# Optimization experiments

Hardware: AMD Instinct MI355X
Metric: run time of the kernel (lower is better)

Reference implementation:

```python
import jax, jax.numpy as jnp
import numpy as np

NEG_SLOPE = 0.2

def gat_conv(x, W, a_src, a_dst, bias, src, dst, num_nodes, concat):
    # x: [N, F_in]; W: [F_in, H*C]; a_src/a_dst: [H, C]; src/dst: [E] (self-loops included)
    H, C = a_src.shape
    h = (x @ W).reshape(-1, H, C)                      # [N, H, C]
    alpha_s = jnp.einsum('nhc,hc->nh', h, a_src)       # [N, H]
    alpha_d = jnp.einsum('nhc,hc->nh', h, a_dst)       # [N, H]
    e = jax.nn.leaky_relu(alpha_s[src] + alpha_d[dst], NEG_SLOPE)  # [E, H]
    # segment softmax over destination nodes
    m = jax.ops.segment_max(e, dst, num_segments=num_nodes)        # [N, H]
    ex = jnp.exp(e - m[dst])
    denom = jax.ops.segment_sum(ex, dst, num_segments=num_nodes)   # [N, H]
    alpha = ex / (denom[dst] + 1e-16)                  # [E, H]
    msg = alpha[:, :, None] * h[src]                   # [E, H, C]
    out = jax.ops.segment_sum(msg, dst, num_segments=num_nodes)    # [N, H, C]
    if concat:
        out = out.reshape(num_nodes, H * C)
    else:
        out = out.mean(axis=1)
    return out + bias

def setup_inputs() -> dict:
    key = jax.random.key(0)
    ks = jax.random.split(key, 12)
    N, F_in, E = 100000, 512, 3200000
    H1, C1 = 8, 8
    OUT = 40
    x = jax.random.normal(ks[0], (N, F_in), dtype=jnp.float32)
    edge_index = jax.random.randint(ks[1], (2, E), 0, N, dtype=jnp.int64)
    glorot = lambda k, shape: jax.random.uniform(k, shape, jnp.float32, -1.0, 1.0) * np.sqrt(6.0 / (shape[0] + shape[-1]))
    W1 = glorot(ks[2], (F_in, H1 * C1))
    a_src1 = glorot(ks[3], (H1, C1))
    a_dst1 = glorot(ks[4], (H1, C1))
    b1 = jnp.zeros((H1 * C1,), jnp.float32)
    W2 = glorot(ks[5], (H1 * C1, OUT))
    a_src2 = glorot(ks[6], (1, OUT))
    a_dst2 = glorot(ks[7], (1, OUT))
    b2 = jnp.zeros((OUT,), jnp.float32)
    return {"x": x, "edge_index": edge_index, "W1": W1, "a_src1": a_src1,
            "a_dst1": a_dst1, "b1": b1, "W2": W2, "a_src2": a_src2,
            "a_dst2": a_dst2, "b2": b2}

def reference(x, edge_index, W1, a_src1, a_dst1, b1, W2, a_src2, a_dst2, b2):
    N = x.shape[0]
    loop = jnp.arange(N, dtype=edge_index.dtype)
    src = jnp.concatenate([edge_index[0], loop])  # add_self_loops=True (PyG default)
    dst = jnp.concatenate([edge_index[1], loop])
    # dropout is identity in eval mode
    h = gat_conv(x, W1, a_src1, a_dst1, b1, src, dst, N, concat=True)   # [N, 64]
    h = jax.nn.elu(h)
    out = gat_conv(h, W2, a_src2, a_dst2, b2, src, dst, N, concat=False)  # [N, 40]
    return out
```

## Files before the change

### kernel.cpp

```cpp
#include <hip/hip_runtime.h>
#include <hip/hip_bf16.h>


typedef __attribute__((ext_vector_type(8))) short short8;
typedef __attribute__((ext_vector_type(4))) short short4v;
typedef __attribute__((ext_vector_type(4))) float float4v;

#define NEG_SLOPE 0.2f

static __device__ __forceinline__ short f2bf(float v){
    union { float f; unsigned u; } x; x.f = v;
    unsigned r = x.u + 0x7fffu + ((x.u >> 16) & 1u);
    return (short)(r >> 16);
}
static __device__ __forceinline__ float bf2f(short s){
    union { unsigned u; float f; } x; x.u = ((unsigned)(unsigned short)s) << 16;
    return x.f;
}

__global__ void pack_w1(const float* __restrict__ W1, short* __restrict__ Bhi, short* __restrict__ Blo){
    int idx = blockIdx.x*blockDim.x + threadIdx.x;
    if (idx >= 64*512) return;
    int j    = idx & 7;
    int lane = (idx >> 3) & 63;
    int ct   = (idx >> 9) & 3;
    int tks  = idx >> 11;
    int ks = tks & 1, t = tks >> 1;
    int m = lane & 15, q = lane >> 4;
    int n = ct*16 + m;
    int k = t*64 + ks*32 + q*8 + j;
    float w = W1[k*64 + n];
    short h = f2bf(w);
    Bhi[idx] = h;
    Blo[idx] = f2bf(w - bf2f(h));
}

__global__ void detect_i64(const int* __restrict__ ei, int* __restrict__ flag){
    __shared__ int any;
    if (threadIdx.x == 0) any = 0;
    __syncthreads();
    if (ei[2*threadIdx.x + 1] != 0) atomicAdd(&any, 1);
    __syncthreads();
    if (threadIdx.x == 0) flag[0] = (any == 0) ? 1 : 0;
}

__global__ __launch_bounds__(256, 4) void gemm1(const float* __restrict__ x,
        const short* __restrict__ Bhi, const short* __restrict__ Blo,
        const float* __restrict__ aS1, const float* __restrict__ aD1,
        short* __restrict__ h1b, float* __restrict__ as1, float* __restrict__ ad1, int N){
    __shared__ __align__(16) float As[2][64][68];
    int tid = threadIdx.x;
    int wave = tid >> 6, lane = tid & 63;
    int m = lane & 15, q = lane >> 4;
    int rowbase = blockIdx.x*64;

    const short8* Bh = (const short8*)Bhi;
    const short8* Bl = (const short8*)Blo;

    int srow[4]; int scol[4];
    #pragma unroll
    for (int i = 0; i < 4; ++i){
        int f = i*256 + tid;
        int r = rowbase + (f >> 4);
        srow[i] = (r < N) ? r : (N-1);
        scol[i] = (f & 15) * 4;
    }

    float4 reg[4];
    #pragma unroll
    for (int i = 0; i < 4; ++i)
        reg[i] = *(const float4*)(x + (size_t)srow[i]*512 + scol[i]);
    #pragma unroll
    for (int i = 0; i < 4; ++i){
        int f = i*256 + tid;
        *(float4*)&As[0][f >> 4][scol[i]] = reg[i];
    }
    __syncthreads();

    float4v acc[4] = {};
    for (int t = 0; t < 8; ++t){
        int cur = t & 1;
        if (t < 7){
            #pragma unroll
            for (int i = 0; i < 4; ++i)
                reg[i] = *(const float4*)(x + (size_t)srow[i]*512 + (t+1)*64 + scol[i]);
        }
        const float* arow = &As[cur][wave*16 + m][0];
        #pragma unroll
        for (int ks = 0; ks < 2; ++ks){
            float v[8];
            *(float4*)&v[0] = *(const float4*)(arow + ks*32 + q*8);
            *(float4*)&v[4] = *(const float4*)(arow + ks*32 + q*8 + 4);
            short8 ahi, alo;
            #pragma unroll
            for (int j = 0; j < 8; ++j){
                union { float f; unsigned u; } tt; tt.f = v[j];
                ahi[j] = (short)(tt.u >> 16);
                union { unsigned u; float f; } th; th.u = tt.u & 0xffff0000u;
                alo[j] = f2bf(v[j] - th.f);
            }
            int fb = ((t*2 + ks)*4)*64 + lane;
            #pragma unroll
            for (int ct = 0; ct < 4; ++ct){
                short8 bhi = Bh[fb + ct*64];
                short8 blo = Bl[fb + ct*64];
                acc[ct] = __builtin_amdgcn_mfma_f32_16x16x32_bf16(ahi, bhi, acc[ct], 0, 0, 0);
                acc[ct] = __builtin_amdgcn_mfma_f32_16x16x32_bf16(ahi, blo, acc[ct], 0, 0, 0);
                acc[ct] = __builtin_amdgcn_mfma_f32_16x16x32_bf16(alo, bhi, acc[ct], 0, 0, 0);
            }
        }
        if (t < 7){
            #pragma unroll
            for (int i = 0; i < 4; ++i){
                int f = i*256 + tid;
                *(float4*)&As[t & 1 ? 0 : 1][f >> 4][scol[i]] = reg[i];
            }
            __syncthreads();
        }
    }

    float* cw = &As[0][0][0] + wave*(16*68);
    #pragma unroll
    for (int ct = 0; ct < 4; ++ct)
        #pragma unroll
        for (int r = 0; r < 4; ++r)
            cw[(q*4+r)*68 + ct*16 + m] = acc[ct][r];

    int row_l = lane >> 2;
    int cseg  = (lane & 3) * 16;
    int gr = rowbase + wave*16 + row_l;
    float vals[16];
    #pragma unroll
    for (int i = 0; i < 4; ++i)
        *(float4*)&vals[i*4] = *(const float4*)&cw[row_l*68 + cseg + i*4];
    if (gr < N){
        short8 o0, o1;
        #pragma unroll
        for (int j = 0; j < 8; ++j){ o0[j] = f2bf(vals[j]); o1[j] = f2bf(vals[8+j]); }
        *(short8*)&h1b[(size_t)gr*64 + cseg]     = o0;
        *(short8*)&h1b[(size_t)gr*64 + cseg + 8] = o1;
        int h0 = (lane & 3) * 2;
        float s0 = 0.f, d0 = 0.f, s1 = 0.f, d1 = 0.f;
        #pragma unroll
        for (int c = 0; c < 8; ++c){
            s0 = fmaf(vals[c],   aS1[h0*8+c],     s0);
            d0 = fmaf(vals[c],   aD1[h0*8+c],     d0);
            s1 = fmaf(vals[8+c], aS1[(h0+1)*8+c], s1);
            d1 = fmaf(vals[8+c], aD1[(h0+1)*8+c], d1);
        }
        float2 sv; sv.x = s0; sv.y = s1;
        float2 dv; dv.x = d0; dv.y = d1;
        *(float2*)&as1[(size_t)gr*8 + h0] = sv;
        *(float2*)&ad1[(size_t)gr*8 + h0] = dv;
    }
}

__global__ __launch_bounds__(256) void bucket_hist(const int* __restrict__ ei,
        const int* __restrict__ flag, int* __restrict__ bhist, int E, int Etot, int K){
    extern __shared__ int hist[];
    for (int i = threadIdx.x; i < K; i += 256) hist[i] = 0;
    __syncthreads();
    int f = flag[0];
    int e0 = blockIdx.x*8192, e1 = min(e0 + 8192, Etot);
    for (int e = e0 + threadIdx.x; e < e1; e += 256){
        int dst = (e < E) ? ei[((size_t)(E + e)) << f] : (e - E);
        atomicAdd(&hist[dst >> 8], 1);
    }
    __syncthreads();
    for (int i = threadIdx.x; i < K; i += 256)
        if (hist[i]) atomicAdd(&bhist[i], hist[i]);
}

__global__ __launch_bounds__(1024) void bucket_scan(const int* __restrict__ bhist,
        int* __restrict__ bbase, int* __restrict__ bcursor, int K){
    __shared__ int s[1024];
    int t = threadIdx.x;
    int v = (t < K) ? bhist[t] : 0;
    s[t] = v; __syncthreads();
    for (int off = 1; off < 1024; off <<= 1){
        int x = (t >= off) ? s[t-off] : 0;
        __syncthreads();
        s[t] += x;
        __syncthreads();
    }
    if (t < K){ int excl = s[t] - v; bbase[t] = excl; bcursor[t] = excl; }
    if (t == K) bbase[K] = s[t];
}

__global__ __launch_bounds__(256) void bucket_place(const int* __restrict__ ei,
        const int* __restrict__ flag, int* __restrict__ bcursor,
        int* __restrict__ staging, int E, int Etot, int K){
    extern __shared__ int sm[];
    int* hist = sm;
    int* base = sm + K;
    for (int i = threadIdx.x; i < K; i += 256) hist[i] = 0;
    __syncthreads();
    int f = flag[0];
    int e0 = blockIdx.x*8192, e1 = min(e0 + 8192, Etot);
    for (int e = e0 + threadIdx.x; e < e1; e += 256){
        int dst = (e < E) ? ei[((size_t)(E + e)) << f] : (e - E);
        atomicAdd(&hist[dst >> 8], 1);
    }
    __syncthreads();
    for (int i = threadIdx.x; i < K; i += 256){
        int c = hist[i];
        base[i] = c ? atomicAdd(&bcursor[i], c) : 0;
        hist[i] = 0;
    }
    __syncthreads();
    for (int e = e0 + threadIdx.x; e < e1; e += 256){
        int src, dst;
        if (e < E){ src = ei[((size_t)e) << f]; dst = ei[((size_t)(E + e)) << f]; }
        else      { src = dst = e - E; }
        int k = dst >> 8;
        int r = atomicAdd(&hist[k], 1);
        staging[base[k] + r] = (src << 8) | (dst & 255);
    }
}

__global__ __launch_bounds__(256) void bucket_csr(const int* __restrict__ staging,
        const int* __restrict__ bbase, int* __restrict__ offs, int* __restrict__ deg,
        int* __restrict__ csr, int N, int K){
    __shared__ int dcnt[256], sc[256], cur[256];
    int k = blockIdx.x, t = threadIdx.x;
    dcnt[t] = 0;
    __syncthreads();
    int s0 = bbase[k], s1 = bbase[k+1];
    for (int i = s0 + t; i < s1; i += 256)
        atomicAdd(&dcnt[staging[i] & 255], 1);
    __syncthreads();
    int v = dcnt[t];
    sc[t] = v; __syncthreads();
    for (int off = 1; off < 256; off <<= 1){
        int x = (t >= off) ? sc[t-off] : 0;
        __syncthreads();
        sc[t] += x;
        __syncthreads();
    }
    int excl = sc[t] - v;
    int node = (k << 8) + t;
    if (node < N){ offs[node] = s0 + excl; deg[node] = v; }
    cur[t] = excl;
    __syncthreads();
    for (int i = s0 + t; i < s1; i += 256){
        int ent = staging[i];
        int p = atomicAdd(&cur[ent & 255], 1);
        csr[s0 + p] = ent >> 8;
    }
}

__global__ __launch_bounds__(256) void agg1(const short* __restrict__ h1b,
        const float* __restrict__ as1, const float* __restrict__ ad1,
        const int* __restrict__ offs, const int* __restrict__ deg, const int* __restrict__ csr,
        const float* __restrict__ b1, short* __restrict__ x1b, int N){
    int w = blockIdx.x*4 + (threadIdx.x >> 6);
    if (w >= N) return;
    int lane = threadIdx.x & 63, h = lane >> 3;
    int s0 = offs[w], d = deg[w];
    float ad = ad1[w*8 + h];
    float l = 0.f, acc = 0.f;
    int i = 0;
    for (; i + 4 <= d; i += 4){
        int sa = csr[s0+i], sb = csr[s0+i+1], sc = csr[s0+i+2], sd = csr[s0+i+3];
        float ea = as1[sa*8+h], eb = as1[sb*8+h], ec = as1[sc*8+h], ed = as1[sd*8+h];
        float va = bf2f(h1b[(size_t)sa*64 + lane]);
        float vb = bf2f(h1b[(size_t)sb*64 + lane]);
        float vc = bf2f(h1b[(size_t)sc*64 + lane]);
        float vd = bf2f(h1b[(size_t)sd*64 + lane]);
        ea += ad; ea = (ea > 0.f) ? ea : NEG_SLOPE*ea; float pa = __expf(ea);
        eb += ad; eb = (eb > 0.f) ? eb : NEG_SLOPE*eb; float pb = __expf(eb);
        ec += ad; ec = (ec > 0.f) ? ec : NEG_SLOPE*ec; float pc = __expf(ec);
        ed += ad; ed = (ed > 0.f) ? ed : NEG_SLOPE*ed; float pd = __expf(ed);
        l += (pa + pb) + (pc + pd);
        acc = fmaf(pa, va, acc); acc = fmaf(pb, vb, acc);
        acc = fmaf(pc, vc, acc); acc = fmaf(pd, vd, acc);
    }
    for (; i < d; ++i){
        int s = csr[s0 + i];
        float e = as1[s*8 + h] + ad;
        e = (e > 0.f) ? e : NEG_SLOPE*e;
        float p = __expf(e);
        l += p;
        acc = fmaf(p, bf2f(h1b[(size_t)s*64 + lane]), acc);
    }
    float o = acc/(l + 1e-16f) + b1[lane];
    o = (o > 0.f) ? o : (__expf(o) - 1.f);
    x1b[(size_t)w*64 + lane] = f2bf(o);
}

__global__ __launch_bounds__(256) void gemm2a(const short* __restrict__ x1b,
        const float* __restrict__ W2, const float* __restrict__ aS2, const float* __restrict__ aD2,
        short* __restrict__ h2b, float* __restrict__ as2, float* __restrict__ ad2, int N){
    __shared__ float w2s[64*40];
    __shared__ float xs[4][64];
    int tid = threadIdx.x;
    for (int i = tid; i < 64*40; i += 256) w2s[i] = W2[i];
    int wv = tid >> 6, lane = tid & 63;
    int n = blockIdx.x*4 + wv;
    bool valid = n < N;
    if (valid && lane < 16){
        short4v xv = *(const short4v*)&x1b[(size_t)n*64 + lane*4];
        xs[wv][lane*4+0] = bf2f(xv[0]);
        xs[wv][lane*4+1] = bf2f(xv[1]);
        xs[wv][lane*4+2] = bf2f(xv[2]);
        xs[wv][lane*4+3] = bf2f(xv[3]);
    }
    __syncthreads();
    int c = (lane < 40) ? lane : 39;
    float acc = 0.f;
    #pragma unroll 8
    for (int k = 0; k < 64; ++k)
        acc = fmaf(xs[wv][k], w2s[k*40 + c], acc);
    float s = (lane < 40) ? acc * aS2[lane] : 0.f;
    float d = (lane < 40) ? acc * aD2[lane] : 0.f;
    #pragma unroll
    for (int off = 32; off > 0; off >>= 1){ s += __shfl_down(s, off, 64); d += __shfl_down(d, off, 64); }
    if (valid){
        if (lane < 40) h2b[(size_t)n*40 + lane] = f2bf(acc);
        if (lane == 0){ as2[n] = s; ad2[n] = d; }
    }
}

__global__ __launch_bounds__(256) void agg2(const short* __restrict__ h2b,
        const float* __restrict__ as2, const float* __restrict__ ad2,
        const int* __restrict__ offs, const int* __restrict__ deg, const int* __restrict__ csr,
        const float* __restrict__ b2, float* __restrict__ out, int N){
    int w = blockIdx.x*4 + (threadIdx.x >> 6);
    if (w >= N) return;
    int lane = threadIdx.x & 63;
    int c = (lane < 40) ? lane : 0;
    int s0 = offs[w], d = deg[w];
    float ad = ad2[w];
    float l = 0.f, acc = 0.f;
    int i = 0;
    for (; i + 4 <= d; i += 4){
        int sa = csr[s0+i], sb = csr[s0+i+1], sc = csr[s0+i+2], sd = csr[s0+i+3];
        float ea = as2[sa], eb = as2[sb], ec = as2[sc], ed = as2[sd];
        float va = bf2f(h2b[(size_t)sa*40 + c]);
        float vb = bf2f(h2b[(size_t)sb*40 + c]);
        float vc = bf2f(h2b[(size_t)sc*40 + c]);
        float vd = bf2f(h2b[(size_t)sd*40 + c]);
        ea += ad; ea = (ea > 0.f) ? ea : NEG_SLOPE*ea; float pa = __expf(ea);
        eb += ad; eb = (eb > 0.f) ? eb : NEG_SLOPE*eb; float pb = __expf(eb);
        ec += ad; ec = (ec > 0.f) ? ec : NEG_SLOPE*ec; float pc = __expf(ec);
        ed += ad; ed = (ed > 0.f) ? ed : NEG_SLOPE*ed; float pd = __expf(ed);
        l += (pa + pb) + (pc + pd);
        acc = fmaf(pa, va, acc); acc = fmaf(pb, vb, acc);
        acc = fmaf(pc, vc, acc); acc = fmaf(pd, vd, acc);
    }
    for (; i < d; ++i){
        int s = csr[s0 + i];
        float e = as2[s] + ad;
        e = (e > 0.f) ? e : NEG_SLOPE*e;
        float p = __expf(e);
        l += p;
        acc = fmaf(p, bf2f(h2b[(size_t)s*40 + c]), acc);
    }
    if (lane < 40) out[(size_t)w*40 + lane] = acc/(l + 1e-16f) + b2[lane];
}

extern "C" void kernel_launch(void* const* d_in, const int* in_sizes, int n_in,
                              void* d_out, int out_size, void* d_ws, size_t ws_size,
                              hipStream_t stream) {
    const float* x    = (const float*)d_in[0];
    const int*   ei   = (const int*)d_in[1];
    const float* W1   = (const float*)d_in[2];
    const float* aS1  = (const float*)d_in[3];
    const float* aD1  = (const float*)d_in[4];
    const float* b1   = (const float*)d_in[5];
    const float* W2   = (const float*)d_in[6];
    const float* aS2  = (const float*)d_in[7];
    const float* aD2  = (const float*)d_in[8];
    const float* b2   = (const float*)d_in[9];
    float* out = (float*)d_out;

    const int N    = in_sizes[0] / 512;
    const int E    = in_sizes[1] / 2;
    const int Etot = E + N;
    const int K    = (N + 255) >> 8;
    const int nAB  = (Etot + 8191) / 8192;

    char* p = (char*)d_ws;
    auto carve = [&](size_t bytes)->char*{ char* q = p; p += ((bytes + 255) & ~(size_t)255); return q; };
    short* h1b   = (short*)carve((size_t)N*64*2);
    short* x1b   = (short*)carve((size_t)N*64*2);
    short* h2b   = (short*)carve((size_t)N*40*2);
    float* as1   = (float*)carve((size_t)N*8*4);
    float* ad1   = (float*)carve((size_t)N*8*4);
    float* as2   = (float*)carve((size_t)N*4);
    float* ad2   = (float*)carve((size_t)N*4);
    int*   deg   = (int*)carve((size_t)N*4);
    int*   offs  = (int*)carve((size_t)N*4);
    int*   bhist = (int*)carve((size_t)(K+1)*4);
    int*   bbase = (int*)carve((size_t)(K+1)*4);
    int*   bcursor=(int*)carve((size_t)(K+1)*4);
    int*   flag  = (int*)carve(256);
    short* Bhi   = (short*)carve(64*512*2);
    short* Blo   = (short*)carve(64*512*2);
    int*   csr   = (int*)carve((size_t)Etot*4);
    int*   staging = (int*)carve((size_t)Etot*4);

    hipMemsetAsync(bhist, 0, (size_t)K*4, stream);

    detect_i64<<<1, 1024, 0, stream>>>(ei, flag);
    pack_w1<<<(64*512 + 255)/256, 256, 0, stream>>>(W1, Bhi, Blo);

    bucket_hist <<<nAB, 256, (size_t)K*4,   stream>>>(ei, flag, bhist, E, Etot, K);
    bucket_scan <<<1, 1024, 0,              stream>>>(bhist, bbase, bcursor, K);
    bucket_place<<<nAB, 256, (size_t)2*K*4, stream>>>(ei, flag, bcursor, staging, E, Etot, K);
    bucket_csr  <<<K, 256, 0,               stream>>>(staging, bbase, offs, deg, csr, N, K);

    gemm1 <<<(N + 63)/64, 256, 0, stream>>>(x, Bhi, Blo, aS1, aD1, h1b, as1, ad1, N);

    agg1  <<<(N + 3)/4,  256, 0, stream>>>(h1b, as1, ad1, offs, deg, csr, b1, x1b, N);
    gemm2a<<<(N + 3)/4,  256, 0, stream>>>(x1b, W2, aS2, aD2, h2b, as2, ad2, N);
    agg2  <<<(N + 3)/4,  256, 0, stream>>>(h2b, as2, ad2, offs, deg, csr, b2, out, N);
}
```

Before: 783.1 us.

## Process each destination node with 16 lanes using 4-wide bf16 vector gathers

Both aggregation kernels now assign 16 threads per destination node instead of a full 64-lane wavefront, with each thread loading four bf16 features at once (short4v) and keeping four accumulators. This puts four nodes in each wavefront, so the per-edge index loads, attention-score loads and exp work are spread over more nodes per instruction and idle lanes in the 40-wide second layer are reduced. The trade-off is more registers per thread and a wider spread of per-wavefront degree, since the wave's loop runs until its highest-degree node is done.

Measured after the change: 696.4 us. -11.1%, faster.

```diff
diff --git a/kernel.cpp b/kernel.cpp
--- a/kernel.cpp
+++ b/kernel.cpp
@@ -253,39 +253,56 @@
         const float* __restrict__ as1, const float* __restrict__ ad1,
         const int* __restrict__ offs, const int* __restrict__ deg, const int* __restrict__ csr,
         const float* __restrict__ b1, short* __restrict__ x1b, int N){
-    int w = blockIdx.x*4 + (threadIdx.x >> 6);
-    if (w >= N) return;
-    int lane = threadIdx.x & 63, h = lane >> 3;
-    int s0 = offs[w], d = deg[w];
-    float ad = ad1[w*8 + h];
-    float l = 0.f, acc = 0.f;
-    int i = 0;
-    for (; i + 4 <= d; i += 4){
-        int sa = csr[s0+i], sb = csr[s0+i+1], sc = csr[s0+i+2], sd = csr[s0+i+3];
-        float ea = as1[sa*8+h], eb = as1[sb*8+h], ec = as1[sc*8+h], ed = as1[sd*8+h];
-        float va = bf2f(h1b[(size_t)sa*64 + lane]);
-        float vb = bf2f(h1b[(size_t)sb*64 + lane]);
-        float vc = bf2f(h1b[(size_t)sc*64 + lane]);
-        float vd = bf2f(h1b[(size_t)sd*64 + lane]);
-        ea += ad; ea = (ea > 0.f) ? ea : NEG_SLOPE*ea; float pa = __expf(ea);
-        eb += ad; eb = (eb > 0.f) ? eb : NEG_SLOPE*eb; float pb = __expf(eb);
-        ec += ad; ec = (ec > 0.f) ? ec : NEG_SLOPE*ec; float pc = __expf(ec);
-        ed += ad; ed = (ed > 0.f) ? ed : NEG_SLOPE*ed; float pd = __expf(ed);
-        l += (pa + pb) + (pc + pd);
-        acc = fmaf(pa, va, acc); acc = fmaf(pb, vb, acc);
-        acc = fmaf(pc, vc, acc); acc = fmaf(pd, vd, acc);
-    }
-    for (; i < d; ++i){
-        int s = csr[s0 + i];
-        float e = as1[s*8 + h] + ad;
-        e = (e > 0.f) ? e : NEG_SLOPE*e;
-        float p = __expf(e);
-        l += p;
-        acc = fmaf(p, bf2f(h1b[(size_t)s*64 + lane]), acc);
-    }
-    float o = acc/(l + 1e-16f) + b1[lane];
-    o = (o > 0.f) ? o : (__expf(o) - 1.f);
-    x1b[(size_t)w*64 + lane] = f2bf(o);
+    int w = blockIdx.x*16 + (threadIdx.x >> 4);
+    if (w < N){
+        int r = threadIdx.x & 15;
+        int h = r >> 1;
+        int f0 = r*4;
+        int s0 = offs[w], d = deg[w];
+        float ad = ad1[w*8 + h];
+        float l = 0.f;
+        float4v acc = {};
+        int i = 0;
+        for (; i + 4 <= d; i += 4){
+            int sa = csr[s0+i], sb = csr[s0+i+1], sc = csr[s0+i+2], sd = csr[s0+i+3];
+            float ea = as1[sa*8+h], eb = as1[sb*8+h], ec = as1[sc*8+h], ed = as1[sd*8+h];
+            short4v va = *(const short4v*)&h1b[(size_t)sa*64 + f0];
+            short4v vb = *(const short4v*)&h1b[(size_t)sb*64 + f0];
+            short4v vc = *(const short4v*)&h1b[(size_t)sc*64 + f0];
+            short4v vd = *(const short4v*)&h1b[(size_t)sd*64 + f0];
+            ea += ad; ea = (ea > 0.f) ? ea : NEG_SLOPE*ea; float pa = __expf(ea);
+            eb += ad; eb = (eb > 0.f) ? eb : NEG_SLOPE*eb; float pb = __expf(eb);
+            ec += ad; ec = (ec > 0.f) ? ec : NEG_SLOPE*ec; float pc = __expf(ec);
+            ed += ad; ed = (ed > 0.f) ? ed : NEG_SLOPE*ed; float pd = __expf(ed);
+            l += (pa + pb) + (pc + pd);
+            #pragma unroll
+            for (int j = 0; j < 4; ++j){
+                acc[j] = fmaf(pa, bf2f(va[j]), acc[j]);
+                acc[j] = fmaf(pb, bf2f(vb[j]), acc[j]);
+                acc[j] = fmaf(pc, bf2f(vc[j]), acc[j]);
+                acc[j] = fmaf(pd, bf2f(vd[j]), acc[j]);
+            }
+        }
+        for (; i < d; ++i){
+            int s = csr[s0 + i];
+            float e = as1[s*8 + h] + ad;
+            e = (e > 0.f) ? e : NEG_SLOPE*e;
+            float p = __expf(e);
+            l += p;
+            short4v v = *(const short4v*)&h1b[(size_t)s*64 + f0];
+            #pragma unroll
+            for (int j = 0; j < 4; ++j)
+                acc[j] = fmaf(p, bf2f(v[j]), acc[j]);
+        }
+        short4v o;
+        #pragma unroll
+        for (int j = 0; j < 4; ++j){
+            float ov = acc[j]/(l + 1e-16f) + b1[f0+j];
+            ov = (ov > 0.f) ? ov : (__expf(ov) - 1.f);
+            o[j] = f2bf(ov);
+        }
+        *(short4v*)&x1b[(size_t)w*64 + f0] = o;
+    }
 }
 
 __global__ __launch_bounds__(256) void gemm2a(const short* __restrict__ x1b,
@@ -325,38 +342,56 @@
         const float* __restrict__ as2, const float* __restrict__ ad2,
         const int* __restrict__ offs, const int* __restrict__ deg, const int* __restrict__ csr,
         const float* __restrict__ b2, float* __restrict__ out, int N){
-    int w = blockIdx.x*4 + (threadIdx.x >> 6);
-    if (w >= N) return;
-    int lane = threadIdx.x & 63;
-    int c = (lane < 40) ? lane : 0;
-    int s0 = offs[w], d = deg[w];
-    float ad = ad2[w];
-    float l = 0.f, acc = 0.f;
-    int i = 0;
-    for (; i + 4 <= d; i += 4){
-        int sa = csr[s0+i], sb = csr[s0+i+1], sc = csr[s0+i+2], sd = csr[s0+i+3];
-        float ea = as2[sa], eb = as2[sb], ec = as2[sc], ed = as2[sd];
-        float va = bf2f(h2b[(size_t)sa*40 + c]);
-        float vb = bf2f(h2b[(size_t)sb*40 + c]);
-        float vc = bf2f(h2b[(size_t)sc*40 + c]);
-        float vd = bf2f(h2b[(size_t)sd*40 + c]);
-        ea += ad; ea = (ea > 0.f) ? ea : NEG_SLOPE*ea; float pa = __expf(ea);
-        eb += ad; eb = (eb > 0.f) ? eb : NEG_SLOPE*eb; float pb = __expf(eb);
-        ec += ad; ec = (ec > 0.f) ? ec : NEG_SLOPE*ec; float pc = __expf(ec);
-        ed += ad; ed = (ed > 0.f) ? ed : NEG_SLOPE*ed; float pd = __expf(ed);
-        l += (pa + pb) + (pc + pd);
-        acc = fmaf(pa, va, acc); acc = fmaf(pb, vb, acc);
-        acc = fmaf(pc, vc, acc); acc = fmaf(pd, vd, acc);
-    }
-    for (; i < d; ++i){
-        int s = csr[s0 + i];
-        float e = as2[s] + ad;
-        e = (e > 0.f) ? e : NEG_SLOPE*e;
-        float p = __expf(e);
-        l += p;
-        acc = fmaf(p, bf2f(h2b[(size_t)s*40 + c]), acc);
-    }
-    if (lane < 40) out[(size_t)w*40 + lane] = acc/(l + 1e-16f) + b2[lane];
+    int w = blockIdx.x*16 + (threadIdx.x >> 4);
+    if (w < N){
+        int r = threadIdx.x & 15;
+        bool pay = r < 10;
+        int f0 = pay ? r*4 : 0;
+        int s0 = offs[w], d = deg[w];
+        float ad = ad2[w];
+        float l = 0.f;
+        float4v acc = {};
+        int i = 0;
+        for (; i + 4 <= d; i += 4){
+            int sa = csr[s0+i], sb = csr[s0+i+1], sc = csr[s0+i+2], sd = csr[s0+i+3];
+            float ea = as2[sa], eb = as2[sb], ec = as2[sc], ed = as2[sd];
+            short4v va = *(const short4v*)&h2b[(size_t)sa*40 + f0];
+            short4v vb = *(const short4v*)&h2b[(size_t)sb*40 + f0];
+            short4v vc = *(const short4v*)&h2b[(size_t)sc*40 + f0];
+            short4v vd = *(const short4v*)&h2b[(size_t)sd*40 + f0];
+            ea += ad; ea = (ea > 0.f) ? ea : NEG_SLOPE*ea; float pa = __expf(ea);
+            eb += ad; eb = (eb > 0.f) ? eb : NEG_SLOPE*eb; float pb = __expf(eb);
+            ec += ad; ec = (ec > 0.f) ? ec : NEG_SLOPE*ec; float pc = __expf(ec);
+            ed += ad; ed = (ed > 0.f) ? ed : NEG_SLOPE*ed; float pd = __expf(ed);
+            l += (pa + pb) + (pc + pd);
+            #pragma unroll
+            for (int j = 0; j < 4; ++j){
+                acc[j] = fmaf(pa, bf2f(va[j]), acc[j]);
+                acc[j] = fmaf(pb, bf2f(vb[j]), acc[j]);
+                acc[j] = fmaf(pc, bf2f(vc[j]), acc[j]);
+                acc[j] = fmaf(pd, bf2f(vd[j]), acc[j]);
+            }
+        }
+        for (; i < d; ++i){
+            int s = csr[s0 + i];
+            float e = as2[s] + ad;
+            e = (e > 0.f) ? e : NEG_SLOPE*e;
+            float p = __expf(e);
+            l += p;
+            short4v v = *(const short4v*)&h2b[(size_t)s*40 + f0];
+            #pragma unroll
+            for (int j = 0; j < 4; ++j)
+                acc[j] = fmaf(p, bf2f(v[j]), acc[j]);
+        }
+        if (pay){
+            float4 o;
+            o.x = acc[0]/(l + 1e-16f) + b2[f0+0];
+            o.y = acc[1]/(l + 1e-16f) + b2[f0+1];
+            o.z = acc[2]/(l + 1e-16f) + b2[f0+2];
+            o.w = acc[3]/(l + 1e-16f) + b2[f0+3];
+            *(float4*)&out[(size_t)w*40 + f0] = o;
+        }
+    }
 }
 
 extern "C" void kernel_launch(void* const* d_in, const int* in_sizes, int n_in,
@@ -412,7 +447,7 @@
 
     gemm1 <<<(N + 63)/64, 256, 0, stream>>>(x, Bhi, Blo, aS1, aD1, h1b, as1, ad1, N);
 
-    agg1  <<<(N + 3)/4,  256, 0, stream>>>(h1b, as1, ad1, offs, deg, csr, b1, x1b, N);
-    gemm2a<<<(N + 3)/4,  256, 0, stream>>>(x1b, W2, aS2, aD2, h2b, as2, ad2, N);
-    agg2  <<<(N + 3)/4,  256, 0, stream>>>(h2b, as2, ad2, offs, deg, csr, b2, out, N);
-}
+    agg1  <<<(N + 15)/16, 256, 0, stream>>>(h1b, as1, ad1, offs, deg, csr, b1, x1b, N);
+    gemm2a<<<(N + 3)/4,   256, 0, stream>>>(x1b, W2, aS2, aD2, h2b, as2, ad2, N);
+    agg2  <<<(N + 15)/16, 256, 0, stream>>>(h2b, as2, ad2, offs, deg, csr, b2, out, N);
+}
```
